# Kernel optimization log

Measured on AMD Instinct MI355X. Metric: run time of the kernel, lower is better.

Reference implementation:

```python
import jax, jax.numpy as jnp
import numpy as np

EPS = 1e-8


def _l2_normalize(x, eps=EPS):
    n = jnp.linalg.norm(x, axis=-1, keepdims=True)
    return x / jnp.maximum(n, eps)


def setup_inputs() -> dict:
    key = jax.random.key(0)
    k1, k2, k3 = jax.random.split(key, 3)
    N_s, N_q, D, C = 65536, 131072, 256, 512
    return {
        "support_features": jax.random.normal(k1, (N_s, D), dtype=jnp.float32),
        "support_labels": jax.random.randint(k2, (N_s,), 0, C, dtype=jnp.int64),
        "query_features": jax.random.normal(k3, (N_q, D), dtype=jnp.float32),
        "logit_scale": jnp.asarray(5.0, dtype=jnp.float32),
        "proto_shrink": jnp.asarray(-2.0, dtype=jnp.float32),
        "num_classes": C,
    }


def reference(support_features, support_labels, query_features, logit_scale, proto_shrink, num_classes):
    # L2-normalize features
    s = _l2_normalize(support_features)            # [N_s, D]
    q = _l2_normalize(query_features)              # [N_q, D]

    labels = support_labels.astype(jnp.int32)
    # per-class segment mean (replaces the python unique/mask loop)
    sums = jax.ops.segment_sum(s, labels, num_segments=num_classes)        # [C, D]
    counts = jax.ops.segment_sum(jnp.ones((s.shape[0],), s.dtype), labels,
                                 num_segments=num_classes)                 # [C]
    counts = jnp.maximum(counts, 1.0)
    class_means = sums / counts[:, None]                                   # [C, D]

    global_centroid = jnp.mean(s, axis=0, keepdims=True)                    # [1, D]

    alpha_base = jnp.clip(jax.nn.sigmoid(proto_shrink), 0.0, 0.4)
    alpha = (alpha_base / jnp.sqrt(counts))[:, None]                        # [C, 1]
    prototypes = (1.0 - alpha) * class_means + alpha * global_centroid
    prototypes = _l2_normalize(prototypes)                                  # [C, D]

    scale = jnp.clip(logit_scale, 1.0, 100.0)
    logits = q @ prototypes.T * scale                                       # [N_q, C]
    unique_classes = jnp.arange(num_classes, dtype=jnp.int32)
    return logits, unique_classes
```

## Files before the change

### kernel.cpp

```cpp
#include <hip/hip_runtime.h>

typedef __attribute__((ext_vector_type(4)))  float f32x4;
typedef __attribute__((ext_vector_type(16))) float f32x16;
typedef __attribute__((ext_vector_type(8)))  short short8;

#define DD 256
#define CC 512
#define LDP2 264

__device__ __forceinline__ unsigned short f2bf(float f) {
    union { float f; unsigned u; } x; x.f = f;
    unsigned r = x.u + 0x7FFFu + ((x.u >> 16) & 1u);
    return (unsigned short)(r >> 16);
}

__device__ __forceinline__ f32x4 ntload4(const f32x4* p) {
    return __builtin_nontemporal_load(p);
}

__global__ __launch_bounds__(256) void class_sum_kernel(
    const f32x4* __restrict__ S, const int* __restrict__ labels,
    float* __restrict__ sums2, float* __restrict__ counts2, int N_s)
{
    const int c = blockIdx.x >> 1, half = blockIdx.x & 1;
    const int w = threadIdx.x >> 6, l = threadIdx.x & 63;
    const int seg  = N_s >> 3;
    const int base = half * (N_s >> 1) + w * seg;
    const int4* lab4 = (const int4*)(labels + base);
    const int iters = seg >> 8;

    float ax = 0.f, ay = 0.f, az = 0.f, aw = 0.f;
    int cnt = 0;

    int4 pf0 = lab4[l];
    int4 pf1 = (iters > 1) ? lab4[64 + l] : make_int4(-1, -1, -1, -1);

    for (int it = 0; it < iters; ++it) {
        int4 lv = pf0;
        pf0 = pf1;
        pf1 = (it + 2 < iters) ? lab4[(it + 2) * 64 + l] : make_int4(-1, -1, -1, -1);
        #pragma unroll
        for (int s = 0; s < 4; ++s) {
            int lab = (s == 0) ? lv.x : (s == 1) ? lv.y : (s == 2) ? lv.z : lv.w;
            unsigned long long m = __ballot(lab == c);
            cnt += __popcll(m);
            while (m) {
                int p0 = __ffsll((long long)m) - 1; m &= m - 1;
                int p1 = -1, p2 = -1, p3 = -1;
                if (m) { p1 = __ffsll((long long)m) - 1; m &= m - 1;
                    if (m) { p2 = __ffsll((long long)m) - 1; m &= m - 1;
                        if (m) { p3 = __ffsll((long long)m) - 1; m &= m - 1; } } }
                f32x4 v0 = ntload4(&S[(size_t)(base + (it * 64 + p0) * 4 + s) * 64 + l]);
                f32x4 v1 = {0,0,0,0}, v2 = {0,0,0,0}, v3 = {0,0,0,0};
                if (p1 >= 0) v1 = ntload4(&S[(size_t)(base + (it * 64 + p1) * 4 + s) * 64 + l]);
                if (p2 >= 0) v2 = ntload4(&S[(size_t)(base + (it * 64 + p2) * 4 + s) * 64 + l]);
                if (p3 >= 0) v3 = ntload4(&S[(size_t)(base + (it * 64 + p3) * 4 + s) * 64 + l]);
                float s0 = v0[0]*v0[0] + v0[1]*v0[1] + v0[2]*v0[2] + v0[3]*v0[3];
                float s1 = v1[0]*v1[0] + v1[1]*v1[1] + v1[2]*v1[2] + v1[3]*v1[3];
                float s2 = v2[0]*v2[0] + v2[1]*v2[1] + v2[2]*v2[2] + v2[3]*v2[3];
                float s3 = v3[0]*v3[0] + v3[1]*v3[1] + v3[2]*v3[2] + v3[3]*v3[3];
                #pragma unroll
                for (int off = 32; off; off >>= 1) {
                    s0 += __shfl_xor(s0, off);
                    s1 += __shfl_xor(s1, off);
                    s2 += __shfl_xor(s2, off);
                    s3 += __shfl_xor(s3, off);
                }
                float i0 = 1.0f / fmaxf(sqrtf(s0), 1e-8f);
                ax += v0[0]*i0; ay += v0[1]*i0; az += v0[2]*i0; aw += v0[3]*i0;
                if (p1 >= 0) { float i1 = 1.0f / fmaxf(sqrtf(s1), 1e-8f);
                    ax += v1[0]*i1; ay += v1[1]*i1; az += v1[2]*i1; aw += v1[3]*i1; }
                if (p2 >= 0) { float i2 = 1.0f / fmaxf(sqrtf(s2), 1e-8f);
                    ax += v2[0]*i2; ay += v2[1]*i2; az += v2[2]*i2; aw += v2[3]*i2; }
                if (p3 >= 0) { float i3 = 1.0f / fmaxf(sqrtf(s3), 1e-8f);
                    ax += v3[0]*i3; ay += v3[1]*i3; az += v3[2]*i3; aw += v3[3]*i3; }
            }
        }
    }

    __shared__ float lred[4][DD];
    __shared__ float lcnt[4];
    lred[w][4*l+0] = ax; lred[w][4*l+1] = ay; lred[w][4*l+2] = az; lred[w][4*l+3] = aw;
    if (l == 0) lcnt[w] = (float)cnt;
    __syncthreads();
    int t = threadIdx.x;
    sums2[(size_t)(half * CC + c) * DD + t] = lred[0][t] + lred[1][t] + lred[2][t] + lred[3][t];
    if (t == 0) counts2[half * CC + c] = lcnt[0] + lcnt[1] + lcnt[2] + lcnt[3];
}

__global__ __launch_bounds__(256) void centroid_kernel(
    const float* __restrict__ sums2, float* __restrict__ gpart)
{
    const int d = threadIdx.x, b = blockIdx.x;
    float s = 0.f;
    for (int j = 0; j < 64; ++j) {
        int c = b * 64 + j;
        s += sums2[(size_t)c * DD + d] + sums2[(size_t)(CC + c) * DD + d];
    }
    gpart[b * DD + d] = s;
}

__global__ __launch_bounds__(256) void proto_kernel(
    const float* __restrict__ sums2, const float* __restrict__ counts2,
    const float* __restrict__ gpart, const float* __restrict__ proto_shrink,
    const float* __restrict__ logit_scale,
    unsigned short* __restrict__ Pt, float* __restrict__ outUC, int N_s)
{
    const int c = blockIdx.x, d = threadIdx.x;
    float ps = proto_shrink[0];
    float ab = 1.0f / (1.0f + __expf(-ps));
    ab = fminf(fmaxf(ab, 0.0f), 0.4f);
    const float sc = fminf(fmaxf(logit_scale[0], 1.0f), 100.0f);

    float sum  = sums2[(size_t)c * DD + d] + sums2[(size_t)(CC + c) * DD + d];
    float cntv = fmaxf(counts2[c] + counts2[CC + c], 1.0f);
    float g = 0.f;
    #pragma unroll
    for (int b = 0; b < 8; ++b) g += gpart[b * DD + d];
    g /= (float)N_s;

    float mean  = sum / cntv;
    float alpha = ab / sqrtf(cntv);
    float p = (1.0f - alpha) * mean + alpha * g;

    float ss = p * p;
    #pragma unroll
    for (int off = 32; off; off >>= 1) ss += __shfl_xor(ss, off);
    __shared__ float l4[4];
    if ((threadIdx.x & 63) == 0) l4[threadIdx.x >> 6] = ss;
    __syncthreads();
    ss = l4[0] + l4[1] + l4[2] + l4[3];
    float inv = sc / fmaxf(sqrtf(ss), 1e-8f);

    const int CT = c >> 5, KT = d >> 4;
    const int lane = (c & 31) + 32 * ((d >> 3) & 1);
    const int e = d & 7;
    Pt[(size_t)(((CT * 16 + KT) * 64 + lane)) * 8 + e] = f2bf(p * inv);
    if (d == 0) outUC[c] = (float)c;
}

__global__ __launch_bounds__(1024, 4) void logits_kernel(
    const float4* __restrict__ Q, const unsigned short* __restrict__ Pt,
    float* __restrict__ out, int nch)
{
    __shared__ unsigned short A[2][64 * LDP2];

    const int t  = threadIdx.x;
    const int w  = t >> 6, l = t & 63;
    const int lr = l & 31, lh = l >> 5;
    const int m0 = blockIdx.x * nch * 64;
    const int sr = t >> 4, sc = t & 15;

    short8 b[16];
    #pragma unroll
    for (int k = 0; k < 16; ++k)
        b[k] = *(const short8*)(Pt + (size_t)((w * 16 + k) * 64 + l) * 8);

    const float4* qbase = Q + (size_t)(m0 + sr) * 64 + sc * 4;

    float4 v[4];
    #pragma unroll
    for (int i = 0; i < 4; ++i) v[i] = qbase[i];

    {
        float ss = 0.f;
        #pragma unroll
        for (int i = 0; i < 4; ++i)
            ss += v[i].x*v[i].x + v[i].y*v[i].y + v[i].z*v[i].z + v[i].w*v[i].w;
        ss += __shfl_xor(ss, 1); ss += __shfl_xor(ss, 2);
        ss += __shfl_xor(ss, 4); ss += __shfl_xor(ss, 8);
        float inv = 1.0f / fmaxf(sqrtf(ss), 1e-8f);
        unsigned short* dst = &A[0][sr * LDP2 + sc * 16];
        #pragma unroll
        for (int h = 0; h < 2; ++h) {
            short8 pk;
            float4 x = v[2*h], y = v[2*h+1];
            pk[0] = (short)f2bf(x.x*inv); pk[1] = (short)f2bf(x.y*inv);
            pk[2] = (short)f2bf(x.z*inv); pk[3] = (short)f2bf(x.w*inv);
            pk[4] = (short)f2bf(y.x*inv); pk[5] = (short)f2bf(y.y*inv);
            pk[6] = (short)f2bf(y.z*inv); pk[7] = (short)f2bf(y.w*inv);
            *(short8*)(dst + h * 8) = pk;
        }
    }
    if (nch > 1) {
        const float4* src = qbase + (size_t)64 * 64;
        #pragma unroll
        for (int i = 0; i < 4; ++i) v[i] = src[i];
    }
    __builtin_amdgcn_sched_barrier(0);
    asm volatile("s_waitcnt lgkmcnt(0)");
    __builtin_amdgcn_sched_barrier(0);
    __builtin_amdgcn_s_barrier();
    __builtin_amdgcn_sched_barrier(0);

    for (int c = 0; c < nch; ++c) {
        const int p = c & 1;

        if (c + 1 < nch) {
            float ss = 0.f;
            #pragma unroll
            for (int i = 0; i < 4; ++i)
                ss += v[i].x*v[i].x + v[i].y*v[i].y + v[i].z*v[i].z + v[i].w*v[i].w;
            ss += __shfl_xor(ss, 1); ss += __shfl_xor(ss, 2);
            ss += __shfl_xor(ss, 4); ss += __shfl_xor(ss, 8);
            float inv = 1.0f / fmaxf(sqrtf(ss), 1e-8f);
            unsigned short* dst = &A[p ^ 1][sr * LDP2 + sc * 16];
            #pragma unroll
            for (int h = 0; h < 2; ++h) {
                short8 pk;
                float4 x = v[2*h], y = v[2*h+1];
                pk[0] = (short)f2bf(x.x*inv); pk[1] = (short)f2bf(x.y*inv);
                pk[2] = (short)f2bf(x.z*inv); pk[3] = (short)f2bf(x.w*inv);
                pk[4] = (short)f2bf(y.x*inv); pk[5] = (short)f2bf(y.y*inv);
                pk[6] = (short)f2bf(y.z*inv); pk[7] = (short)f2bf(y.w*inv);
                *(short8*)(dst + h * 8) = pk;
            }
            if (c + 2 < nch) {
                const float4* src = qbase + (size_t)(c + 2) * 64 * 64;
                #pragma unroll
                for (int i = 0; i < 4; ++i) v[i] = src[i];
            }
        }

        #pragma unroll
        for (int st = 0; st < 2; ++st) {
            f32x16 acc;
            #pragma unroll
            for (int r = 0; r < 16; ++r) acc[r] = 0.f;
            const unsigned short* ab = &A[p][(st * 32 + lr) * LDP2 + lh * 8];
            __builtin_amdgcn_s_setprio(1);
            #pragma unroll
            for (int k = 0; k < 16; ++k) {
                short8 af = *(const short8*)(ab + k * 16);
                acc = __builtin_amdgcn_mfma_f32_32x32x16_bf16(af, b[k], acc, 0, 0, 0);
            }
            __builtin_amdgcn_s_setprio(0);
            const int col = 32 * w + lr;
            const int rb  = m0 + c * 64 + st * 32 + 4 * lh;
            #pragma unroll
            for (int r = 0; r < 16; ++r) {
                int row = rb + (r & 3) + 8 * (r >> 2);
                __builtin_nontemporal_store(acc[r], &out[(size_t)row * CC + col]);
            }
        }

        __builtin_amdgcn_sched_barrier(0);
        asm volatile("s_waitcnt lgkmcnt(0)");
        __builtin_amdgcn_sched_barrier(0);
        __builtin_amdgcn_s_barrier();
        __builtin_amdgcn_sched_barrier(0);
    }
}

extern "C" void kernel_launch(void* const* d_in, const int* in_sizes, int n_in,
                              void* d_out, int out_size, void* d_ws, size_t ws_size,
                              hipStream_t stream) {
    const float* S      = (const float*)d_in[0];
    const int*   labels = (const int*)d_in[1];
    const float* Qf     = (const float*)d_in[2];
    const float* lscale = (const float*)d_in[3];
    const float* pshr   = (const float*)d_in[4];

    const int N_s = in_sizes[0] / DD;
    const int N_q = in_sizes[2] / DD;

    float* sums2         = (float*)d_ws;
    float* counts2       = (float*)((char*)d_ws + 1048576);
    float* gpart         = (float*)((char*)d_ws + 1052672);
    unsigned short* Pt   = (unsigned short*)((char*)d_ws + 1060864);

    float* out   = (float*)d_out;
    float* outUC = out + (size_t)N_q * CC;

    const int nblk = 256;
    const int nch  = N_q / (nblk * 64);

    class_sum_kernel<<<2 * CC, 256, 0, stream>>>((const f32x4*)S, labels, sums2, counts2, N_s);
    centroid_kernel<<<8, 256, 0, stream>>>(sums2, gpart);
    proto_kernel<<<CC, 256, 0, stream>>>(sums2, counts2, gpart, pshr, lscale, Pt, outUC, N_s);
    logits_kernel<<<nblk, 1024, 0, stream>>>((const float4*)Qf, Pt, out, nch);
}
```

Before: 110.5 us.

## Fuse class-sum, centroid, prototype and logits into one cooperative kernel

Replaces the four separate launches with a single cooperative kernel of 256 blocks × 1024 threads. Each block first computes the per-class sums for two classes, then meets the others at a grid sync. After that every block reduces the global centroid, builds its two prototype rows into the bf16 layout and meets the others at a second grid sync. Only then does it run the MFMA logits loop. This removes inter-kernel launch gaps and overlaps the first query-chunk load and normalization with the class-sum phase. In exchange it pays for two grid-wide barriers, and every block redundantly re-reads the 512×256 sums to form the centroid.

```diff
diff --git a/kernel.cpp b/kernel.cpp
--- a/kernel.cpp
+++ b/kernel.cpp
@@ -1,4 +1,7 @@
 #include <hip/hip_runtime.h>
+#include <hip/hip_cooperative_groups.h>
+
+namespace cg = cooperative_groups;
 
 typedef __attribute__((ext_vector_type(4)))  float f32x4;
 typedef __attribute__((ext_vector_type(16))) float f32x16;
@@ -18,149 +21,109 @@
     return __builtin_nontemporal_load(p);
 }
 
-__global__ __launch_bounds__(256) void class_sum_kernel(
-    const f32x4* __restrict__ S, const int* __restrict__ labels,
-    float* __restrict__ sums2, float* __restrict__ counts2, int N_s)
-{
-    const int c = blockIdx.x >> 1, half = blockIdx.x & 1;
-    const int w = threadIdx.x >> 6, l = threadIdx.x & 63;
-    const int seg  = N_s >> 3;
-    const int base = half * (N_s >> 1) + w * seg;
-    const int4* lab4 = (const int4*)(labels + base);
-    const int iters = seg >> 8;
-
-    float ax = 0.f, ay = 0.f, az = 0.f, aw = 0.f;
-    int cnt = 0;
-
-    int4 pf0 = lab4[l];
-    int4 pf1 = (iters > 1) ? lab4[64 + l] : make_int4(-1, -1, -1, -1);
-
-    for (int it = 0; it < iters; ++it) {
-        int4 lv = pf0;
-        pf0 = pf1;
-        pf1 = (it + 2 < iters) ? lab4[(it + 2) * 64 + l] : make_int4(-1, -1, -1, -1);
-        #pragma unroll
-        for (int s = 0; s < 4; ++s) {
-            int lab = (s == 0) ? lv.x : (s == 1) ? lv.y : (s == 2) ? lv.z : lv.w;
-            unsigned long long m = __ballot(lab == c);
-            cnt += __popcll(m);
-            while (m) {
-                int p0 = __ffsll((long long)m) - 1; m &= m - 1;
-                int p1 = -1, p2 = -1, p3 = -1;
-                if (m) { p1 = __ffsll((long long)m) - 1; m &= m - 1;
-                    if (m) { p2 = __ffsll((long long)m) - 1; m &= m - 1;
-                        if (m) { p3 = __ffsll((long long)m) - 1; m &= m - 1; } } }
-                f32x4 v0 = ntload4(&S[(size_t)(base + (it * 64 + p0) * 4 + s) * 64 + l]);
-                f32x4 v1 = {0,0,0,0}, v2 = {0,0,0,0}, v3 = {0,0,0,0};
-                if (p1 >= 0) v1 = ntload4(&S[(size_t)(base + (it * 64 + p1) * 4 + s) * 64 + l]);
-                if (p2 >= 0) v2 = ntload4(&S[(size_t)(base + (it * 64 + p2) * 4 + s) * 64 + l]);
-                if (p3 >= 0) v3 = ntload4(&S[(size_t)(base + (it * 64 + p3) * 4 + s) * 64 + l]);
-                float s0 = v0[0]*v0[0] + v0[1]*v0[1] + v0[2]*v0[2] + v0[3]*v0[3];
-                float s1 = v1[0]*v1[0] + v1[1]*v1[1] + v1[2]*v1[2] + v1[3]*v1[3];
-                float s2 = v2[0]*v2[0] + v2[1]*v2[1] + v2[2]*v2[2] + v2[3]*v2[3];
-                float s3 = v3[0]*v3[0] + v3[1]*v3[1] + v3[2]*v3[2] + v3[3]*v3[3];
-                #pragma unroll
-                for (int off = 32; off; off >>= 1) {
-                    s0 += __shfl_xor(s0, off);
-                    s1 += __shfl_xor(s1, off);
-                    s2 += __shfl_xor(s2, off);
-                    s3 += __shfl_xor(s3, off);
-                }
-                float i0 = 1.0f / fmaxf(sqrtf(s0), 1e-8f);
-                ax += v0[0]*i0; ay += v0[1]*i0; az += v0[2]*i0; aw += v0[3]*i0;
-                if (p1 >= 0) { float i1 = 1.0f / fmaxf(sqrtf(s1), 1e-8f);
-                    ax += v1[0]*i1; ay += v1[1]*i1; az += v1[2]*i1; aw += v1[3]*i1; }
-                if (p2 >= 0) { float i2 = 1.0f / fmaxf(sqrtf(s2), 1e-8f);
-                    ax += v2[0]*i2; ay += v2[1]*i2; az += v2[2]*i2; aw += v2[3]*i2; }
-                if (p3 >= 0) { float i3 = 1.0f / fmaxf(sqrtf(s3), 1e-8f);
-                    ax += v3[0]*i3; ay += v3[1]*i3; az += v3[2]*i3; aw += v3[3]*i3; }
-            }
-        }
-    }
-
-    __shared__ float lred[4][DD];
-    __shared__ float lcnt[4];
-    lred[w][4*l+0] = ax; lred[w][4*l+1] = ay; lred[w][4*l+2] = az; lred[w][4*l+3] = aw;
-    if (l == 0) lcnt[w] = (float)cnt;
-    __syncthreads();
-    int t = threadIdx.x;
-    sums2[(size_t)(half * CC + c) * DD + t] = lred[0][t] + lred[1][t] + lred[2][t] + lred[3][t];
-    if (t == 0) counts2[half * CC + c] = lcnt[0] + lcnt[1] + lcnt[2] + lcnt[3];
-}
-
-__global__ __launch_bounds__(256) void centroid_kernel(
-    const float* __restrict__ sums2, float* __restrict__ gpart)
-{
-    const int d = threadIdx.x, b = blockIdx.x;
-    float s = 0.f;
-    for (int j = 0; j < 64; ++j) {
-        int c = b * 64 + j;
-        s += sums2[(size_t)c * DD + d] + sums2[(size_t)(CC + c) * DD + d];
-    }
-    gpart[b * DD + d] = s;
-}
-
-__global__ __launch_bounds__(256) void proto_kernel(
-    const float* __restrict__ sums2, const float* __restrict__ counts2,
-    const float* __restrict__ gpart, const float* __restrict__ proto_shrink,
-    const float* __restrict__ logit_scale,
-    unsigned short* __restrict__ Pt, float* __restrict__ outUC, int N_s)
-{
-    const int c = blockIdx.x, d = threadIdx.x;
-    float ps = proto_shrink[0];
-    float ab = 1.0f / (1.0f + __expf(-ps));
-    ab = fminf(fmaxf(ab, 0.0f), 0.4f);
-    const float sc = fminf(fmaxf(logit_scale[0], 1.0f), 100.0f);
-
-    float sum  = sums2[(size_t)c * DD + d] + sums2[(size_t)(CC + c) * DD + d];
-    float cntv = fmaxf(counts2[c] + counts2[CC + c], 1.0f);
-    float g = 0.f;
-    #pragma unroll
-    for (int b = 0; b < 8; ++b) g += gpart[b * DD + d];
-    g /= (float)N_s;
-
-    float mean  = sum / cntv;
-    float alpha = ab / sqrtf(cntv);
-    float p = (1.0f - alpha) * mean + alpha * g;
-
-    float ss = p * p;
-    #pragma unroll
-    for (int off = 32; off; off >>= 1) ss += __shfl_xor(ss, off);
-    __shared__ float l4[4];
-    if ((threadIdx.x & 63) == 0) l4[threadIdx.x >> 6] = ss;
-    __syncthreads();
-    ss = l4[0] + l4[1] + l4[2] + l4[3];
-    float inv = sc / fmaxf(sqrtf(ss), 1e-8f);
-
-    const int CT = c >> 5, KT = d >> 4;
-    const int lane = (c & 31) + 32 * ((d >> 3) & 1);
-    const int e = d & 7;
-    Pt[(size_t)(((CT * 16 + KT) * 64 + lane)) * 8 + e] = f2bf(p * inv);
-    if (d == 0) outUC[c] = (float)c;
-}
-
-__global__ __launch_bounds__(1024, 4) void logits_kernel(
-    const float4* __restrict__ Q, const unsigned short* __restrict__ Pt,
-    float* __restrict__ out, int nch)
+__global__ __launch_bounds__(1024, 4) void fused_kernel(
+    const float4* __restrict__ Q, const f32x4* __restrict__ S,
+    const int* __restrict__ labels, const float* __restrict__ logit_scale,
+    const float* __restrict__ proto_shrink,
+    float* __restrict__ sums_g, unsigned short* __restrict__ Pt,
+    float* __restrict__ out, int N_s, int N_q, int nch)
 {
     __shared__ unsigned short A[2][64 * LDP2];
-
+    __shared__ float lred[16][DD];
+    __shared__ float lcnt16[16];
+    __shared__ float ccnt[2];
+    __shared__ float centq[4][DD];
+    __shared__ float l4c[2][4];
+
+    const int b  = blockIdx.x;
     const int t  = threadIdx.x;
-    const int w  = t >> 6, l = t & 63;
+    const int wv = t >> 6, l = t & 63;
     const int lr = l & 31, lh = l >> 5;
-    const int m0 = blockIdx.x * nch * 64;
+    const int m0 = b * nch * 64;
     const int sr = t >> 4, sc = t & 15;
-
-    short8 b[16];
-    #pragma unroll
-    for (int k = 0; k < 16; ++k)
-        b[k] = *(const short8*)(Pt + (size_t)((w * 16 + k) * 64 + l) * 8);
 
     const float4* qbase = Q + (size_t)(m0 + sr) * 64 + sc * 4;
 
     float4 v[4];
     #pragma unroll
     for (int i = 0; i < 4; ++i) v[i] = qbase[i];
+
+    {
+        const int myc  = 2 * b + (wv >> 3);
+        const int seg  = wv & 7;
+        const int base = seg * (N_s >> 3);
+        const int4* lab4 = (const int4*)(labels + base);
+        const int iters = (N_s >> 3) >> 8;
+
+        float ax = 0.f, ay = 0.f, az = 0.f, aw = 0.f;
+        int cnt = 0;
+
+        int4 pf0 = lab4[l];
+        int4 pf1 = (iters > 1) ? lab4[64 + l] : make_int4(-1, -1, -1, -1);
+
+        for (int it = 0; it < iters; ++it) {
+            int4 lv = pf0;
+            pf0 = pf1;
+            pf1 = (it + 2 < iters) ? lab4[(it + 2) * 64 + l] : make_int4(-1, -1, -1, -1);
+            #pragma unroll
+            for (int s = 0; s < 4; ++s) {
+                int lab = (s == 0) ? lv.x : (s == 1) ? lv.y : (s == 2) ? lv.z : lv.w;
+                unsigned long long m = __ballot(lab == myc);
+                cnt += __popcll(m);
+                while (m) {
+                    int p0 = __ffsll((long long)m) - 1; m &= m - 1;
+                    int p1 = -1, p2 = -1, p3 = -1;
+                    if (m) { p1 = __ffsll((long long)m) - 1; m &= m - 1;
+                        if (m) { p2 = __ffsll((long long)m) - 1; m &= m - 1;
+                            if (m) { p3 = __ffsll((long long)m) - 1; m &= m - 1; } } }
+                    f32x4 v0 = ntload4(&S[(size_t)(base + (it * 64 + p0) * 4 + s) * 64 + l]);
+                    f32x4 v1 = {0,0,0,0}, v2 = {0,0,0,0}, v3 = {0,0,0,0};
+                    if (p1 >= 0) v1 = ntload4(&S[(size_t)(base + (it * 64 + p1) * 4 + s) * 64 + l]);
+                    if (p2 >= 0) v2 = ntload4(&S[(size_t)(base + (it * 64 + p2) * 4 + s) * 64 + l]);
+                    if (p3 >= 0) v3 = ntload4(&S[(size_t)(base + (it * 64 + p3) * 4 + s) * 64 + l]);
+                    float s0 = v0[0]*v0[0] + v0[1]*v0[1] + v0[2]*v0[2] + v0[3]*v0[3];
+                    float s1 = v1[0]*v1[0] + v1[1]*v1[1] + v1[2]*v1[2] + v1[3]*v1[3];
+                    float s2 = v2[0]*v2[0] + v2[1]*v2[1] + v2[2]*v2[2] + v2[3]*v2[3];
+                    float s3 = v3[0]*v3[0] + v3[1]*v3[1] + v3[2]*v3[2] + v3[3]*v3[3];
+                    #pragma unroll
+                    for (int off = 32; off; off >>= 1) {
+                        s0 += __shfl_xor(s0, off);
+                        s1 += __shfl_xor(s1, off);
+                        s2 += __shfl_xor(s2, off);
+                        s3 += __shfl_xor(s3, off);
+                    }
+                    float i0 = 1.0f / fmaxf(sqrtf(s0), 1e-8f);
+                    ax += v0[0]*i0; ay += v0[1]*i0; az += v0[2]*i0; aw += v0[3]*i0;
+                    if (p1 >= 0) { float i1 = 1.0f / fmaxf(sqrtf(s1), 1e-8f);
+                        ax += v1[0]*i1; ay += v1[1]*i1; az += v1[2]*i1; aw += v1[3]*i1; }
+                    if (p2 >= 0) { float i2 = 1.0f / fmaxf(sqrtf(s2), 1e-8f);
+                        ax += v2[0]*i2; ay += v2[1]*i2; az += v2[2]*i2; aw += v2[3]*i2; }
+                    if (p3 >= 0) { float i3 = 1.0f / fmaxf(sqrtf(s3), 1e-8f);
+                        ax += v3[0]*i3; ay += v3[1]*i3; az += v3[2]*i3; aw += v3[3]*i3; }
+                }
+            }
+        }
+
+        lred[wv][4*l+0] = ax; lred[wv][4*l+1] = ay;
+        lred[wv][4*l+2] = az; lred[wv][4*l+3] = aw;
+        if (l == 0) lcnt16[wv] = (float)cnt;
+    }
+    __syncthreads();
+
+    if (t < 512) {
+        const int ci = t >> 8, d = t & 255;
+        float s = 0.f;
+        #pragma unroll
+        for (int vv = 0; vv < 8; ++vv) s += lred[ci * 8 + vv][d];
+        lred[ci][d] = s;
+        sums_g[(size_t)(2 * b + ci) * DD + d] = s;
+    }
+    if (t < 2) {
+        float cs = 0.f;
+        #pragma unroll
+        for (int vv = 0; vv < 8; ++vv) cs += lcnt16[t * 8 + vv];
+        ccnt[t] = cs;
+    }
 
     {
         float ss = 0.f;
@@ -187,11 +150,57 @@
         #pragma unroll
         for (int i = 0; i < 4; ++i) v[i] = src[i];
     }
-    __builtin_amdgcn_sched_barrier(0);
-    asm volatile("s_waitcnt lgkmcnt(0)");
-    __builtin_amdgcn_sched_barrier(0);
-    __builtin_amdgcn_s_barrier();
-    __builtin_amdgcn_sched_barrier(0);
+
+    __threadfence();
+    cg::this_grid().sync();
+
+    {
+        const int d = t & 255, q = t >> 8;
+        float sq = 0.f;
+        for (int j = 0; j < 128; ++j)
+            sq += sums_g[(size_t)(q * 128 + j) * DD + d];
+        centq[q][d] = sq;
+    }
+    __syncthreads();
+
+    if (t < 512) {
+        const int ci = t >> 8, d = t & 255;
+        const int cls = 2 * b + ci;
+        float ps = proto_shrink[0];
+        float abase = 1.0f / (1.0f + __expf(-ps));
+        abase = fminf(fmaxf(abase, 0.0f), 0.4f);
+        const float scl = fminf(fmaxf(logit_scale[0], 1.0f), 100.0f);
+
+        float g = (centq[0][d] + centq[1][d] + centq[2][d] + centq[3][d]) / (float)N_s;
+        float cntv = fmaxf(ccnt[ci], 1.0f);
+        float mean = lred[ci][d] / cntv;
+        float alpha = abase / sqrtf(cntv);
+        float p = (1.0f - alpha) * mean + alpha * g;
+
+        float ss = p * p;
+        #pragma unroll
+        for (int off = 32; off; off >>= 1) ss += __shfl_xor(ss, off);
+        if ((t & 63) == 0) l4c[ci][(t >> 6) & 3] = ss;
+        __syncthreads();
+        ss = l4c[ci][0] + l4c[ci][1] + l4c[ci][2] + l4c[ci][3];
+        float inv = scl / fmaxf(sqrtf(ss), 1e-8f);
+
+        const int CT = cls >> 5, KT = d >> 4;
+        const int lane2 = (cls & 31) + 32 * ((d >> 3) & 1);
+        const int e = d & 7;
+        Pt[(size_t)((CT * 16 + KT) * 64 + lane2) * 8 + e] = f2bf(p * inv);
+        if (b == 0) out[(size_t)N_q * CC + t] = (float)t;
+    } else {
+        __syncthreads();
+    }
+
+    __threadfence();
+    cg::this_grid().sync();
+
+    short8 bfr[16];
+    #pragma unroll
+    for (int k = 0; k < 16; ++k)
+        bfr[k] = *(const short8*)(Pt + (size_t)((wv * 16 + k) * 64 + l) * 8);
 
     for (int c = 0; c < nch; ++c) {
         const int p = c & 1;
@@ -232,10 +241,10 @@
             #pragma unroll
             for (int k = 0; k < 16; ++k) {
                 short8 af = *(const short8*)(ab + k * 16);
-                acc = __builtin_amdgcn_mfma_f32_32x32x16_bf16(af, b[k], acc, 0, 0, 0);
+                acc = __builtin_amdgcn_mfma_f32_32x32x16_bf16(af, bfr[k], acc, 0, 0, 0);
             }
             __builtin_amdgcn_s_setprio(0);
-            const int col = 32 * w + lr;
+            const int col = 32 * wv + lr;
             const int rb  = m0 + c * 64 + st * 32 + 4 * lh;
             #pragma unroll
             for (int r = 0; r < 16; ++r) {
@@ -255,28 +264,24 @@
 extern "C" void kernel_launch(void* const* d_in, const int* in_sizes, int n_in,
                               void* d_out, int out_size, void* d_ws, size_t ws_size,
                               hipStream_t stream) {
-    const float* S      = (const float*)d_in[0];
-    const int*   labels = (const int*)d_in[1];
-    const float* Qf     = (const float*)d_in[2];
-    const float* lscale = (const float*)d_in[3];
-    const float* pshr   = (const float*)d_in[4];
-
-    const int N_s = in_sizes[0] / DD;
-    const int N_q = in_sizes[2] / DD;
-
-    float* sums2         = (float*)d_ws;
-    float* counts2       = (float*)((char*)d_ws + 1048576);
-    float* gpart         = (float*)((char*)d_ws + 1052672);
-    unsigned short* Pt   = (unsigned short*)((char*)d_ws + 1060864);
-
-    float* out   = (float*)d_out;
-    float* outUC = out + (size_t)N_q * CC;
-
-    const int nblk = 256;
-    const int nch  = N_q / (nblk * 64);
-
-    class_sum_kernel<<<2 * CC, 256, 0, stream>>>((const f32x4*)S, labels, sums2, counts2, N_s);
-    centroid_kernel<<<8, 256, 0, stream>>>(sums2, gpart);
-    proto_kernel<<<CC, 256, 0, stream>>>(sums2, counts2, gpart, pshr, lscale, Pt, outUC, N_s);
-    logits_kernel<<<nblk, 1024, 0, stream>>>((const float4*)Qf, Pt, out, nch);
-}
+    const float4* Qf     = (const float4*)d_in[2];
+    const f32x4*  S4     = (const f32x4*)d_in[0];
+    const int*    labels = (const int*)d_in[1];
+    const float*  lscale = (const float*)d_in[3];
+    const float*  pshr   = (const float*)d_in[4];
+
+    int N_s = in_sizes[0] / DD;
+    int N_q = in_sizes[2] / DD;
+
+    float* sums_g        = (float*)d_ws;
+    unsigned short* Pt   = (unsigned short*)((char*)d_ws + 524288);
+    float* outp  = (float*)d_out;
+
+    int nch = N_q / (256 * 64);
+
+    void* args[] = { (void*)&Qf, (void*)&S4, (void*)&labels, (void*)&lscale,
+                     (void*)&pshr, (void*)&sums_g, (void*)&Pt, (void*)&outp,
+                     (void*)&N_s, (void*)&N_q, (void*)&nch };
+    hipLaunchCooperativeKernel((const void*)fused_kernel, dim3(256), dim3(1024),
+                               args, 0, stream);
+}
```

After: 329.4 us. +198.1%, slower.
